# Performance work log

Measured on AMD Instinct MI355X. Metric: run time of the kernel, lower is better.

## Reference

```python
import jax, jax.numpy as jnp
import numpy as np

N_HEAD = 16
WINDOW = 128
CAUSAL = False


def setup_inputs() -> dict:
    key = jax.random.key(0)
    ks = jax.random.split(key, 5)
    B, T, D = 1, 4096, 1024
    x = jax.random.normal(ks[0], (B, T, D), dtype=jnp.float32)
    w_in = jax.random.normal(ks[1], (3 * D, D), dtype=jnp.float32) * 0.02
    b_in = jax.random.normal(ks[2], (3 * D,), dtype=jnp.float32) * 0.02
    w_out = jax.random.normal(ks[3], (D, D), dtype=jnp.float32) * 0.02
    b_out = jax.random.normal(ks[4], (D,), dtype=jnp.float32) * 0.02
    return {"x": x, "w_in": w_in, "b_in": b_in, "w_out": w_out, "b_out": b_out}


def _window_attention(x, w_in, b_in, w_out, b_out):
    B, T, D = x.shape
    H = N_HEAD
    hd = D // H
    scale = 1.0 / jnp.sqrt(jnp.float32(hd))

    # fused in-projection, as in torch nn.MultiheadAttention (y = x @ W^T + b)
    qkv = jnp.einsum('btd,ed->bte', x, w_in) + b_in  # (B, T, 3D)
    q, k, v = jnp.split(qkv, 3, axis=-1)
    # (B, H, T, hd)
    q = q.reshape(B, T, H, hd).transpose(0, 2, 1, 3)
    k = k.reshape(B, T, H, hd).transpose(0, 2, 1, 3)
    v = v.reshape(B, T, H, hd).transpose(0, 2, 1, 3)

    scores = jnp.einsum('bhqd,bhkd->bhqk', q, k) * scale  # (B, H, T, T)

    idx = jnp.arange(T)
    diff = idx[:, None] - idx[None, :]
    if CAUSAL:
        allowed = (diff >= 0) & (diff <= WINDOW)
    else:
        allowed = jnp.abs(diff) <= WINDOW
    NEG = jnp.float32(-1e30)
    scores = jnp.where(allowed[None, None, :, :], scores, NEG)

    attn = jax.nn.softmax(scores, axis=-1)
    ctx = jnp.einsum('bhqk,bhkd->bhqd', attn, v)  # (B, H, T, hd)
    ctx = ctx.transpose(0, 2, 1, 3).reshape(B, T, D)
    out = jnp.einsum('btd,ed->bte', ctx, w_out) + b_out
    return x + out  # residual, as in the module


def reference(x, w_in, b_in, w_out, b_out):
    return _window_attention(x, w_in, b_in, w_out, b_out)
```

## Files before the change

kernel.cpp:

```cpp
#include <hip/hip_runtime.h>

#define T_SEQ 4096
#define DMODEL 1024
#define NHEAD 16
#define HDIM 64
#define WIN 128

typedef __attribute__((ext_vector_type(8))) short bf16x8;
typedef __attribute__((ext_vector_type(4))) float f32x4;
typedef __attribute__((ext_vector_type(4))) unsigned short u16x4;

__device__ __forceinline__ unsigned short f2bf(float f) {
  unsigned int u = __builtin_bit_cast(unsigned int, f);
  return (unsigned short)((u + 0x7fffu + ((u >> 16) & 1u)) >> 16);
}

__device__ __forceinline__ void gload_lds16(const unsigned short* g,
                                            unsigned short* l) {
  __builtin_amdgcn_global_load_lds(
      (const __attribute__((address_space(1))) void*)g,
      (__attribute__((address_space(3))) void*)l, 16, 0, 0);
}

__global__ void convert_f32_bf16(const float* __restrict__ src,
                                 unsigned short* __restrict__ dst, int n4) {
  int stride = gridDim.x * blockDim.x;
  for (int i = blockIdx.x * blockDim.x + threadIdx.x; i < n4; i += stride) {
    float4 v = reinterpret_cast<const float4*>(src)[i];
    u16x4 o;
    o.x = f2bf(v.x); o.y = f2bf(v.y); o.z = f2bf(v.z); o.w = f2bf(v.w);
    reinterpret_cast<u16x4*>(dst)[i] = o;
  }
}

template <int EPI, int BM, int BN>
__global__ __launch_bounds__(256) void gemm_lds(
    const unsigned short* __restrict__ A,
    const unsigned short* __restrict__ B,
    const float* __restrict__ bias,
    unsigned short* __restrict__ q_buf,
    unsigned short* __restrict__ k_buf,
    unsigned short* __restrict__ vt_buf,
    const float* __restrict__ x_res,
    float* __restrict__ out) {
  const int K = DMODEL;
  constexpr int MR = BM / 32, NR = BN / 32;
  constexpr int AL = BM / 64, BL = BN / 64;
  __shared__ __align__(16) unsigned short As[BM * 32];
  __shared__ __align__(16) unsigned short Bs[BN * 32];

  int tid = threadIdx.x;
  int lane = tid & 63;
  int wave = tid >> 6;
  int wr = wave >> 1, wc = wave & 1;
  int lo = lane & 15, hi = lane >> 4;
  int t0 = blockIdx.y * BM;
  int e0 = blockIdx.x * BN;

  f32x4 acc[MR][NR];
#pragma unroll
  for (int m = 0; m < MR; ++m)
#pragma unroll
    for (int n = 0; n < NR; ++n) acc[m][n] = (f32x4){0.f, 0.f, 0.f, 0.f};

  const unsigned short* Aptr[AL];
  const unsigned short* Bptr[BL];
  unsigned short* ldsA[AL];
  unsigned short* ldsB[BL];
#pragma unroll
  for (int l = 0; l < AL; ++l) {
    int i = l * 256 + tid;
    Aptr[l] = A + (size_t)(t0 + (i >> 2)) * K + (i & 3) * 8;
    ldsA[l] = As + l * 2048 + wave * 512;
  }
#pragma unroll
  for (int l = 0; l < BL; ++l) {
    int i = l * 256 + tid;
    Bptr[l] = B + (size_t)(e0 + (i >> 2)) * K + (i & 3) * 8;
    ldsB[l] = Bs + l * 2048 + wave * 512;
  }

  for (int k0 = 0; k0 < K; k0 += 32) {
    __syncthreads();
#pragma unroll
    for (int l = 0; l < AL; ++l) gload_lds16(Aptr[l] + k0, ldsA[l]);
#pragma unroll
    for (int l = 0; l < BL; ++l) gload_lds16(Bptr[l] + k0, ldsB[l]);
    __syncthreads();

    bf16x8 af[MR], bfr[NR];
#pragma unroll
    for (int m = 0; m < MR; ++m)
      af[m] = *reinterpret_cast<const bf16x8*>(
          &As[(wr * (BM / 2) + m * 16 + lo) * 32 + hi * 8]);
#pragma unroll
    for (int n = 0; n < NR; ++n)
      bfr[n] = *reinterpret_cast<const bf16x8*>(
          &Bs[(wc * (BN / 2) + n * 16 + lo) * 32 + hi * 8]);
#pragma unroll
    for (int m = 0; m < MR; ++m)
#pragma unroll
      for (int n = 0; n < NR; ++n)
        acc[m][n] =
            __builtin_amdgcn_mfma_f32_16x16x32_bf16(af[m], bfr[n], acc[m][n], 0, 0, 0);
  }

  int t0w = t0 + wr * (BM / 2);
  int e0w = e0 + wc * (BN / 2);
#pragma unroll
  for (int m = 0; m < MR; ++m) {
#pragma unroll
    for (int n = 0; n < NR; ++n) {
      int e = e0w + n * 16 + lo;
      float bv = bias[e];
#pragma unroll
      for (int j = 0; j < 4; ++j) {
        int t = t0w + m * 16 + hi * 4 + j;
        float val = acc[m][n][j] + bv;
        if (EPI == 0) {
          unsigned short bb = f2bf(val);
          int part = e >> 10;
          int h = (e >> 6) & 15;
          int d = e & 63;
          if (part == 0)
            q_buf[((size_t)h * T_SEQ + t) * HDIM + d] = bb;
          else if (part == 1)
            k_buf[((size_t)h * T_SEQ + t) * HDIM + d] = bb;
          else
            vt_buf[((size_t)(h * HDIM + d)) * T_SEQ + t] = bb;
        } else {
          size_t idx = (size_t)t * DMODEL + e;
          out[idx] = val + x_res[idx];
        }
      }
    }
  }
}

__global__ __launch_bounds__(256) void win_attn(
    const unsigned short* __restrict__ q_buf,
    const unsigned short* __restrict__ k_buf,
    const unsigned short* __restrict__ vt_buf,
    unsigned short* __restrict__ ctx) {
  __shared__ __align__(16) unsigned short p_lds[4][2][16 * 40];
  int tid = threadIdx.x;
  int wave = tid >> 6;
  int lane = tid & 63;
  int lo = lane & 15, hi = lane >> 4;

  int id = blockIdx.x;
  int sw = (id & 7) * (512 / 8) + (id >> 3);
  int job = sw * 4 + wave;
  int h = job >> 7;
  int q0 = (job & 127) * 32;
  const float SC = 0.18033688011112042f;

  bf16x8 aq[2][2];
#pragma unroll
  for (int u = 0; u < 2; ++u) {
    const unsigned short* qrow =
        q_buf + ((size_t)h * T_SEQ + q0 + u * 16 + lo) * HDIM + hi * 8;
    aq[u][0] = *reinterpret_cast<const bf16x8*>(qrow);
    aq[u][1] = *reinterpret_cast<const bf16x8*>(qrow + 32);
  }

  float L[2][4] = {{0.f, 0.f, 0.f, 0.f}, {0.f, 0.f, 0.f, 0.f}};
  f32x4 o[2][4];
#pragma unroll
  for (int u = 0; u < 2; ++u)
#pragma unroll
    for (int n = 0; n < 4; ++n) o[u][n] = (f32x4){0.f, 0.f, 0.f, 0.f};

  int jstart = q0 - WIN; if (jstart < 0) jstart = 0;
  int jend = q0 + 32 + WIN; if (jend > T_SEQ) jend = T_SEQ;

  for (int j0 = jstart; j0 < jend; j0 += 32) {
    bf16x8 bk[2][2];
#pragma unroll
    for (int c = 0; c < 2; ++c) {
      int krow = j0 + c * 16 + lo;
      const unsigned short* kp = k_buf + ((size_t)h * T_SEQ + krow) * HDIM + hi * 8;
      bk[c][0] = *reinterpret_cast<const bf16x8*>(kp);
      bk[c][1] = *reinterpret_cast<const bf16x8*>(kp + 32);
    }
#pragma unroll
    for (int u = 0; u < 2; ++u) {
#pragma unroll
      for (int c = 0; c < 2; ++c) {
        f32x4 z = (f32x4){0.f, 0.f, 0.f, 0.f};
        z = __builtin_amdgcn_mfma_f32_16x16x32_bf16(aq[u][0], bk[c][0], z, 0, 0, 0);
        z = __builtin_amdgcn_mfma_f32_16x16x32_bf16(aq[u][1], bk[c][1], z, 0, 0, 0);
        int kj = j0 + c * 16 + lo;
#pragma unroll
        for (int j = 0; j < 4; ++j) {
          int q = q0 + u * 16 + hi * 4 + j;
          bool ok = (q - kj <= WIN) && (kj - q <= WIN);
          float p = ok ? __builtin_amdgcn_exp2f(z[j] * SC) : 0.f;
          L[u][j] += p;
          p_lds[wave][u][(hi * 4 + j) * 40 + c * 16 + lo] = f2bf(p);
        }
      }
    }
    bf16x8 pa[2];
    pa[0] = *reinterpret_cast<const bf16x8*>(&p_lds[wave][0][lo * 40 + hi * 8]);
    pa[1] = *reinterpret_cast<const bf16x8*>(&p_lds[wave][1][lo * 40 + hi * 8]);
#pragma unroll
    for (int n = 0; n < 4; ++n) {
      const unsigned short* vp =
          vt_buf + ((size_t)(h * HDIM + n * 16 + lo)) * T_SEQ + j0 + hi * 8;
      bf16x8 bv = *reinterpret_cast<const bf16x8*>(vp);
      o[0][n] = __builtin_amdgcn_mfma_f32_16x16x32_bf16(pa[0], bv, o[0][n], 0, 0, 0);
      o[1][n] = __builtin_amdgcn_mfma_f32_16x16x32_bf16(pa[1], bv, o[1][n], 0, 0, 0);
    }
  }
#pragma unroll
  for (int u = 0; u < 2; ++u)
#pragma unroll
    for (int j = 0; j < 4; ++j) {
#pragma unroll
      for (int w = 1; w < 16; w <<= 1) L[u][j] += __shfl_xor(L[u][j], w, 64);
    }
#pragma unroll
  for (int u = 0; u < 2; ++u)
#pragma unroll
    for (int j = 0; j < 4; ++j) {
      int t = q0 + u * 16 + hi * 4 + j;
      float inv = 1.f / L[u][j];
#pragma unroll
      for (int n = 0; n < 4; ++n)
        ctx[(size_t)t * DMODEL + h * HDIM + n * 16 + lo] = f2bf(o[u][n][j] * inv);
    }
}

extern "C" void kernel_launch(void* const* d_in, const int* in_sizes, int n_in,
                              void* d_out, int out_size, void* d_ws, size_t ws_size,
                              hipStream_t stream) {
  const float* x = (const float*)d_in[0];
  const float* w_in = (const float*)d_in[1];
  const float* b_in = (const float*)d_in[2];
  const float* w_out = (const float*)d_in[3];
  const float* b_out = (const float*)d_in[4];
  float* out = (float*)d_out;

  char* ws = (char*)d_ws;
  size_t off = 0;
  auto take = [&](size_t bytes) {
    char* p = ws + off;
    off += (bytes + 255) & ~(size_t)255;
    return p;
  };
  unsigned short* x_bf = (unsigned short*)take((size_t)T_SEQ * DMODEL * 2);
  unsigned short* w_in_bf = (unsigned short*)take((size_t)3 * DMODEL * DMODEL * 2);
  unsigned short* w_out_bf = (unsigned short*)take((size_t)DMODEL * DMODEL * 2);
  unsigned short* q_buf = (unsigned short*)take((size_t)T_SEQ * DMODEL * 2);
  unsigned short* k_buf = (unsigned short*)take((size_t)T_SEQ * DMODEL * 2);
  unsigned short* vt_buf = (unsigned short*)take((size_t)T_SEQ * DMODEL * 2 + 8192);
  unsigned short* ctx = (unsigned short*)take((size_t)T_SEQ * DMODEL * 2);

  convert_f32_bf16<<<2048, 256, 0, stream>>>(x, x_bf, T_SEQ * DMODEL / 4);
  convert_f32_bf16<<<2048, 256, 0, stream>>>(w_in, w_in_bf, 3 * DMODEL * DMODEL / 4);
  convert_f32_bf16<<<1024, 256, 0, stream>>>(w_out, w_out_bf, DMODEL * DMODEL / 4);

  dim3 g1(3 * DMODEL / 128, T_SEQ / 128);
  gemm_lds<0, 128, 128><<<g1, 256, 0, stream>>>(x_bf, w_in_bf, b_in, q_buf, k_buf,
                                                vt_buf, nullptr, nullptr);

  win_attn<<<512, 256, 0, stream>>>(q_buf, k_buf, vt_buf, ctx);

  dim3 g2(DMODEL / 64, T_SEQ / 128);
  gemm_lds<1, 128, 64><<<g2, 256, 0, stream>>>(ctx, w_out_bf, b_out, nullptr, nullptr,
                                               nullptr, x, out);
}
```

Before: 101.2 us.

## Fuse conversions, deepen GEMM K tile with swizzled LDS, prefetch attention K/V

```diff
diff --git a/kernel.cpp b/kernel.cpp
--- a/kernel.cpp
+++ b/kernel.cpp
@@ -22,15 +22,25 @@
       (__attribute__((address_space(3))) void*)l, 16, 0, 0);
 }
 
-__global__ void convert_f32_bf16(const float* __restrict__ src,
-                                 unsigned short* __restrict__ dst, int n4) {
+__global__ void convert_all(const float* __restrict__ x,
+                            const float* __restrict__ w_in,
+                            const float* __restrict__ w_out,
+                            unsigned short* __restrict__ x_bf,
+                            unsigned short* __restrict__ w_in_bf,
+                            unsigned short* __restrict__ w_out_bf) {
   int stride = gridDim.x * blockDim.x;
-  for (int i = blockIdx.x * blockDim.x + threadIdx.x; i < n4; i += stride) {
-    float4 v = reinterpret_cast<const float4*>(src)[i];
-    u16x4 o;
-    o.x = f2bf(v.x); o.y = f2bf(v.y); o.z = f2bf(v.z); o.w = f2bf(v.w);
-    reinterpret_cast<u16x4*>(dst)[i] = o;
-  }
+  int t0 = blockIdx.x * blockDim.x + threadIdx.x;
+#define CVT(SRC, DST, N4)                                          \
+  for (int i = t0; i < (N4); i += stride) {                        \
+    float4 v = reinterpret_cast<const float4*>(SRC)[i];            \
+    u16x4 o;                                                       \
+    o.x = f2bf(v.x); o.y = f2bf(v.y); o.z = f2bf(v.z); o.w = f2bf(v.w); \
+    reinterpret_cast<u16x4*>(DST)[i] = o;                          \
+  }
+  CVT(x, x_bf, T_SEQ * DMODEL / 4)
+  CVT(w_in, w_in_bf, 3 * DMODEL * DMODEL / 4)
+  CVT(w_out, w_out_bf, DMODEL * DMODEL / 4)
+#undef CVT
 }
 
 template <int EPI, int BM, int BN>
@@ -45,9 +55,9 @@
     float* __restrict__ out) {
   const int K = DMODEL;
   constexpr int MR = BM / 32, NR = BN / 32;
-  constexpr int AL = BM / 64, BL = BN / 64;
-  __shared__ __align__(16) unsigned short As[BM * 32];
-  __shared__ __align__(16) unsigned short Bs[BN * 32];
+  constexpr int AL = BM / 32, BL = BN / 32;
+  __shared__ __align__(16) unsigned short As[BM * 64];
+  __shared__ __align__(16) unsigned short Bs[BN * 64];
 
   int tid = threadIdx.x;
   int lane = tid & 63;
@@ -70,17 +80,21 @@
 #pragma unroll
   for (int l = 0; l < AL; ++l) {
     int i = l * 256 + tid;
-    Aptr[l] = A + (size_t)(t0 + (i >> 2)) * K + (i & 3) * 8;
-    ldsA[l] = As + l * 2048 + wave * 512;
+    int row = i >> 3;
+    int c8 = (i & 7) ^ (row & 7);
+    Aptr[l] = A + (size_t)(t0 + row) * K + c8 * 8;
+    ldsA[l] = As + (l * 256 + wave * 64) * 8;
   }
 #pragma unroll
   for (int l = 0; l < BL; ++l) {
     int i = l * 256 + tid;
-    Bptr[l] = B + (size_t)(e0 + (i >> 2)) * K + (i & 3) * 8;
-    ldsB[l] = Bs + l * 2048 + wave * 512;
-  }
-
-  for (int k0 = 0; k0 < K; k0 += 32) {
+    int row = i >> 3;
+    int c8 = (i & 7) ^ (row & 7);
+    Bptr[l] = B + (size_t)(e0 + row) * K + c8 * 8;
+    ldsB[l] = Bs + (l * 256 + wave * 64) * 8;
+  }
+
+  for (int k0 = 0; k0 < K; k0 += 64) {
     __syncthreads();
 #pragma unroll
     for (int l = 0; l < AL; ++l) gload_lds16(Aptr[l] + k0, ldsA[l]);
@@ -88,21 +102,28 @@
     for (int l = 0; l < BL; ++l) gload_lds16(Bptr[l] + k0, ldsB[l]);
     __syncthreads();
 
-    bf16x8 af[MR], bfr[NR];
-#pragma unroll
-    for (int m = 0; m < MR; ++m)
-      af[m] = *reinterpret_cast<const bf16x8*>(
-          &As[(wr * (BM / 2) + m * 16 + lo) * 32 + hi * 8]);
-#pragma unroll
-    for (int n = 0; n < NR; ++n)
-      bfr[n] = *reinterpret_cast<const bf16x8*>(
-          &Bs[(wc * (BN / 2) + n * 16 + lo) * 32 + hi * 8]);
-#pragma unroll
-    for (int m = 0; m < MR; ++m)
-#pragma unroll
-      for (int n = 0; n < NR; ++n)
-        acc[m][n] =
-            __builtin_amdgcn_mfma_f32_16x16x32_bf16(af[m], bfr[n], acc[m][n], 0, 0, 0);
+#pragma unroll
+    for (int ks = 0; ks < 2; ++ks) {
+      bf16x8 af[MR], bfr[NR];
+#pragma unroll
+      for (int m = 0; m < MR; ++m) {
+        int row = wr * (BM / 2) + m * 16 + lo;
+        af[m] = *reinterpret_cast<const bf16x8*>(
+            &As[row * 64 + ((ks * 4 + hi) ^ (row & 7)) * 8]);
+      }
+#pragma unroll
+      for (int n = 0; n < NR; ++n) {
+        int row = wc * (BN / 2) + n * 16 + lo;
+        bfr[n] = *reinterpret_cast<const bf16x8*>(
+            &Bs[row * 64 + ((ks * 4 + hi) ^ (row & 7)) * 8]);
+      }
+#pragma unroll
+      for (int m = 0; m < MR; ++m)
+#pragma unroll
+        for (int n = 0; n < NR; ++n)
+          acc[m][n] = __builtin_amdgcn_mfma_f32_16x16x32_bf16(af[m], bfr[n],
+                                                              acc[m][n], 0, 0, 0);
+    }
   }
 
   int t0w = t0 + wr * (BM / 2);
@@ -113,24 +134,32 @@
     for (int n = 0; n < NR; ++n) {
       int e = e0w + n * 16 + lo;
       float bv = bias[e];
-#pragma unroll
-      for (int j = 0; j < 4; ++j) {
-        int t = t0w + m * 16 + hi * 4 + j;
-        float val = acc[m][n][j] + bv;
-        if (EPI == 0) {
-          unsigned short bb = f2bf(val);
-          int part = e >> 10;
-          int h = (e >> 6) & 15;
-          int d = e & 63;
-          if (part == 0)
-            q_buf[((size_t)h * T_SEQ + t) * HDIM + d] = bb;
-          else if (part == 1)
-            k_buf[((size_t)h * T_SEQ + t) * HDIM + d] = bb;
-          else
-            vt_buf[((size_t)(h * HDIM + d)) * T_SEQ + t] = bb;
+      if (EPI == 0) {
+        int part = e >> 10;
+        int h = (e >> 6) & 15;
+        int d = e & 63;
+        if (part == 2) {
+          int t = t0w + m * 16 + hi * 4;
+          u16x4 pk;
+          pk.x = f2bf(acc[m][n][0] + bv);
+          pk.y = f2bf(acc[m][n][1] + bv);
+          pk.z = f2bf(acc[m][n][2] + bv);
+          pk.w = f2bf(acc[m][n][3] + bv);
+          *reinterpret_cast<u16x4*>(&vt_buf[((size_t)(h * HDIM + d)) * T_SEQ + t]) = pk;
         } else {
+          unsigned short* dst = (part == 0) ? q_buf : k_buf;
+#pragma unroll
+          for (int j = 0; j < 4; ++j) {
+            int t = t0w + m * 16 + hi * 4 + j;
+            dst[((size_t)h * T_SEQ + t) * HDIM + d] = f2bf(acc[m][n][j] + bv);
+          }
+        }
+      } else {
+#pragma unroll
+        for (int j = 0; j < 4; ++j) {
+          int t = t0w + m * 16 + hi * 4 + j;
           size_t idx = (size_t)t * DMODEL + e;
-          out[idx] = val + x_res[idx];
+          out[idx] = acc[m][n][j] + bv + x_res[idx];
         }
       }
     }
@@ -174,22 +203,37 @@
   int jstart = q0 - WIN; if (jstart < 0) jstart = 0;
   int jend = q0 + 32 + WIN; if (jend > T_SEQ) jend = T_SEQ;
 
+  bf16x8 kc[2][2];
+#pragma unroll
+  for (int c = 0; c < 2; ++c) {
+    const unsigned short* kp =
+        k_buf + ((size_t)h * T_SEQ + jstart + c * 16 + lo) * HDIM + hi * 8;
+    kc[c][0] = *reinterpret_cast<const bf16x8*>(kp);
+    kc[c][1] = *reinterpret_cast<const bf16x8*>(kp + 32);
+  }
+
   for (int j0 = jstart; j0 < jend; j0 += 32) {
-    bf16x8 bk[2][2];
+    int jn = (j0 + 32 < jend) ? j0 + 32 : jstart;
+    bf16x8 kn[2][2];
 #pragma unroll
     for (int c = 0; c < 2; ++c) {
-      int krow = j0 + c * 16 + lo;
-      const unsigned short* kp = k_buf + ((size_t)h * T_SEQ + krow) * HDIM + hi * 8;
-      bk[c][0] = *reinterpret_cast<const bf16x8*>(kp);
-      bk[c][1] = *reinterpret_cast<const bf16x8*>(kp + 32);
-    }
+      const unsigned short* kp =
+          k_buf + ((size_t)h * T_SEQ + jn + c * 16 + lo) * HDIM + hi * 8;
+      kn[c][0] = *reinterpret_cast<const bf16x8*>(kp);
+      kn[c][1] = *reinterpret_cast<const bf16x8*>(kp + 32);
+    }
+    bf16x8 bv[4];
+#pragma unroll
+    for (int n = 0; n < 4; ++n)
+      bv[n] = *reinterpret_cast<const bf16x8*>(
+          vt_buf + ((size_t)(h * HDIM + n * 16 + lo)) * T_SEQ + j0 + hi * 8);
 #pragma unroll
     for (int u = 0; u < 2; ++u) {
 #pragma unroll
       for (int c = 0; c < 2; ++c) {
         f32x4 z = (f32x4){0.f, 0.f, 0.f, 0.f};
-        z = __builtin_amdgcn_mfma_f32_16x16x32_bf16(aq[u][0], bk[c][0], z, 0, 0, 0);
-        z = __builtin_amdgcn_mfma_f32_16x16x32_bf16(aq[u][1], bk[c][1], z, 0, 0, 0);
+        z = __builtin_amdgcn_mfma_f32_16x16x32_bf16(aq[u][0], kc[c][0], z, 0, 0, 0);
+        z = __builtin_amdgcn_mfma_f32_16x16x32_bf16(aq[u][1], kc[c][1], z, 0, 0, 0);
         int kj = j0 + c * 16 + lo;
 #pragma unroll
         for (int j = 0; j < 4; ++j) {
@@ -206,11 +250,13 @@
     pa[1] = *reinterpret_cast<const bf16x8*>(&p_lds[wave][1][lo * 40 + hi * 8]);
 #pragma unroll
     for (int n = 0; n < 4; ++n) {
-      const unsigned short* vp =
-          vt_buf + ((size_t)(h * HDIM + n * 16 + lo)) * T_SEQ + j0 + hi * 8;
-      bf16x8 bv = *reinterpret_cast<const bf16x8*>(vp);
-      o[0][n] = __builtin_amdgcn_mfma_f32_16x16x32_bf16(pa[0], bv, o[0][n], 0, 0, 0);
-      o[1][n] = __builtin_amdgcn_mfma_f32_16x16x32_bf16(pa[1], bv, o[1][n], 0, 0, 0);
+      o[0][n] = __builtin_amdgcn_mfma_f32_16x16x32_bf16(pa[0], bv[n], o[0][n], 0, 0, 0);
+      o[1][n] = __builtin_amdgcn_mfma_f32_16x16x32_bf16(pa[1], bv[n], o[1][n], 0, 0, 0);
+    }
+#pragma unroll
+    for (int c = 0; c < 2; ++c) {
+      kc[c][0] = kn[c][0];
+      kc[c][1] = kn[c][1];
     }
   }
 #pragma unroll
@@ -257,9 +303,7 @@
   unsigned short* vt_buf = (unsigned short*)take((size_t)T_SEQ * DMODEL * 2 + 8192);
   unsigned short* ctx = (unsigned short*)take((size_t)T_SEQ * DMODEL * 2);
 
-  convert_f32_bf16<<<2048, 256, 0, stream>>>(x, x_bf, T_SEQ * DMODEL / 4);
-  convert_f32_bf16<<<2048, 256, 0, stream>>>(w_in, w_in_bf, 3 * DMODEL * DMODEL / 4);
-  convert_f32_bf16<<<1024, 256, 0, stream>>>(w_out, w_out_bf, DMODEL * DMODEL / 4);
+  convert_all<<<2048, 256, 0, stream>>>(x, w_in, w_out, x_bf, w_in_bf, w_out_bf);
 
   dim3 g1(3 * DMODEL / 128, T_SEQ / 128);
   gemm_lds<0, 128, 128><<<g1, 256, 0, stream>>>(x_bf, w_in_bf, b_in, q_buf, k_buf,
```

New measurement: 93.38 us. 7.8% less time.
